# Optimization experiments

Measured on AMD Instinct MI355X. Metric: run time of the kernel, lower is better.

Reference implementation:

```python
import jax, jax.numpy as jnp
import numpy as np

# SREChead (single level, width=0.25): stem 1x1 (128->64) + two 3x3 convs (64->64),
# each Conv->BN(eval, folded into scale/shift)->SiLU, then 1x1 reg (4ch) and obj (1ch)
# heads, followed by YOLOX-style grid decode.
B, C_IN, HGT, WID = 64, 128, 80, 80
C_H = 64            # int(256 * 0.25)
STRIDE = 32


def _conv(x, w):
    # NCHW conv, stride 1, SAME padding (pad=(k-1)//2 as in BaseConv)
    return jax.lax.conv_general_dilated(
        x, w, window_strides=(1, 1), padding='SAME',
        dimension_numbers=('NCHW', 'OIHW', 'NCHW'))


def _bn_silu(y, scale, shift):
    # eval-mode BatchNorm folded to per-channel affine, then SiLU
    return jax.nn.silu(y * scale[None, :, None, None] + shift[None, :, None, None])


def setup_inputs() -> dict:
    key = jax.random.key(0)
    ks = jax.random.split(key, 12)

    def w(k, o, i, kh, kw, s=0.05):
        return jax.random.normal(k, (o, i, kh, kw), jnp.float32) * s

    def bn(k, c):
        k1, k2 = jax.random.split(k)
        scale = 1.0 + 0.1 * jax.random.normal(k1, (c,), jnp.float32)
        shift = 0.05 * jax.random.normal(k2, (c,), jnp.float32)
        return scale, shift

    stem_scale, stem_shift = bn(ks[2], C_H)
    c1_scale, c1_shift = bn(ks[4], C_H)
    c2_scale, c2_shift = bn(ks[6], C_H)
    return {
        'x': jax.random.normal(ks[0], (B, C_IN, HGT, WID), jnp.float32),
        'stem_w': w(ks[1], C_H, C_IN, 1, 1),
        'stem_scale': stem_scale, 'stem_shift': stem_shift,
        'c1_w': w(ks[3], C_H, C_H, 3, 3),
        'c1_scale': c1_scale, 'c1_shift': c1_shift,
        'c2_w': w(ks[5], C_H, C_H, 3, 3),
        'c2_scale': c2_scale, 'c2_shift': c2_shift,
        'reg_w': w(ks[7], 4, C_H, 1, 1),
        'reg_b': jnp.zeros((4,), jnp.float32),
        'obj_w': w(ks[8], 1, C_H, 1, 1),
        'obj_b': jnp.zeros((1,), jnp.float32),
    }


def reference(x, stem_w, stem_scale, stem_shift,
              c1_w, c1_scale, c1_shift,
              c2_w, c2_scale, c2_shift,
              reg_w, reg_b, obj_w, obj_b):
    f = _bn_silu(_conv(x, stem_w), stem_scale, stem_shift)       # [B,64,H,W]
    f = _bn_silu(_conv(f, c1_w), c1_scale, c1_shift)
    f = _bn_silu(_conv(f, c2_w), c2_scale, c2_shift)
    reg = _conv(f, reg_w) + reg_b[None, :, None, None]           # [B,4,H,W]
    obj = jax.nn.sigmoid(_conv(f, obj_w) + obj_b[None, :, None, None])  # [B,1,H,W]
    out = jnp.concatenate([reg, obj], axis=1)                    # [B,5,H,W]
    out = out.reshape(out.shape[0], 5, HGT * WID).transpose(0, 2, 1)  # [B,HW,5]
    # YOLOX decode: xy = (pred_xy + grid) * stride, wh = exp(pred_wh) * stride
    yv, xv = jnp.meshgrid(jnp.arange(HGT), jnp.arange(WID), indexing='ij')
    grid = jnp.stack([xv, yv], -1).reshape(1, HGT * WID, 2).astype(out.dtype)
    xy = (out[..., :2] + grid) * STRIDE
    wh = jnp.exp(out[..., 2:4]) * STRIDE
    return jnp.concatenate([xy, wh, out[..., 4:5]], axis=-1)     # [B,HW,5]
```

## Files before the change

kernel.cpp:

```cpp
#include <hip/hip_runtime.h>
#include <cstdint>


typedef short short8 __attribute__((ext_vector_type(8)));
typedef float floatx4 __attribute__((ext_vector_type(4)));

#define NPIX 6400
#define NBATCH 64

static __device__ __forceinline__ unsigned short f2bf(float f) {
    unsigned u = __builtin_bit_cast(unsigned, f);
    u += 0x7fffu + ((u >> 16) & 1u);
    return (unsigned short)(u >> 16);
}

static __device__ __forceinline__ float silu_(float v) {
    return v / (1.0f + __expf(-v));
}

__global__ __launch_bounds__(256) void rearr_w_kernel(
    const float* __restrict__ w1, const float* __restrict__ w2,
    unsigned short* __restrict__ wB1, unsigned short* __restrict__ wB2) {
    int idx = blockIdx.x * 256 + threadIdx.x;
    const float* src = (idx < 36864) ? w1 : w2;
    unsigned short* dst = (idx < 36864) ? wB1 : wB2;
    int e = (idx < 36864) ? idx : idx - 36864;
    int j = e & 7;
    int lane = (e >> 3) & 63;
    int nt = (e >> 9) & 3;
    int kb = e >> 11;
    int co = nt * 16 + (lane & 15);
    int k = kb * 32 + ((lane >> 4) * 8) + j;
    int ci = k & 63;
    int tap = k >> 6;
    dst[e] = f2bf(src[(co * 64 + ci) * 9 + tap]);
}

__global__ __launch_bounds__(256) void stem_kernel(
    const float* __restrict__ x, const float* __restrict__ w,
    const float* __restrict__ scale, const float* __restrict__ shift,
    unsigned short* __restrict__ f1) {
    int b = blockIdx.y;
    int wv = threadIdx.x >> 6;
    int lane = threadIdx.x & 63;
    int l15 = lane & 15, q = lane >> 4;
    int pbase = blockIdx.x * 256 + wv * 64;

    short8 wf[4][4];
    #pragma unroll
    for (int nt = 0; nt < 4; ++nt) {
        int co = nt * 16 + l15;
        #pragma unroll
        for (int kb = 0; kb < 4; ++kb) {
            const float* wp = w + co * 128 + kb * 32 + q * 8;
            short8 f;
            #pragma unroll
            for (int j = 0; j < 8; ++j) f[j] = (short)f2bf(wp[j]);
            wf[nt][kb] = f;
        }
    }
    float sc[4], sh[4];
    #pragma unroll
    for (int nt = 0; nt < 4; ++nt) {
        sc[nt] = scale[nt * 16 + l15];
        sh[nt] = shift[nt * 16 + l15];
    }

    floatx4 acc[4][4];
    floatx4 zf = {0.0f, 0.0f, 0.0f, 0.0f};
    #pragma unroll
    for (int mt = 0; mt < 4; ++mt)
        #pragma unroll
        for (int nt = 0; nt < 4; ++nt) acc[mt][nt] = zf;

    #pragma unroll
    for (int kb = 0; kb < 4; ++kb) {
        short8 af[4];
        #pragma unroll
        for (int mt = 0; mt < 4; ++mt) {
            int p = pbase + mt * 16 + l15;
            const float* xp = x + (b * 128 + kb * 32 + q * 8) * NPIX + p;
            short8 f;
            #pragma unroll
            for (int j = 0; j < 8; ++j) f[j] = (short)f2bf(xp[j * NPIX]);
            af[mt] = f;
        }
        #pragma unroll
        for (int mt = 0; mt < 4; ++mt)
            #pragma unroll
            for (int nt = 0; nt < 4; ++nt)
                acc[mt][nt] = __builtin_amdgcn_mfma_f32_16x16x32_bf16(
                    af[mt], wf[nt][kb], acc[mt][nt], 0, 0, 0);
    }

    #pragma unroll
    for (int mt = 0; mt < 4; ++mt) {
        #pragma unroll
        for (int nt = 0; nt < 4; ++nt) {
            int co = nt * 16 + l15;
            #pragma unroll
            for (int r = 0; r < 4; ++r) {
                int p = pbase + mt * 16 + q * 4 + r;
                float v = acc[mt][nt][r] * sc[nt] + sh[nt];
                f1[(b * NPIX + p) * 64 + co] = f2bf(silu_(v));
            }
        }
    }
}

__global__ __launch_bounds__(256) void conv3_kernel(
    const unsigned short* __restrict__ fin, const unsigned short* __restrict__ wB,
    const float* __restrict__ scale, const float* __restrict__ shift,
    unsigned short* __restrict__ fout) {
    int b = blockIdx.y;
    int wv = threadIdx.x >> 6;
    int lane = threadIdx.x & 63;
    int l15 = lane & 15, q = lane >> 4;
    int pbase = blockIdx.x * 256 + wv * 64;

    int py[4], pxl[4];
    #pragma unroll
    for (int mt = 0; mt < 4; ++mt) {
        int pt = pbase + mt * 16;
        py[mt] = pt / 80;
        pxl[mt] = pt % 80 + l15;
    }

    floatx4 acc[4][4];
    floatx4 zf = {0.0f, 0.0f, 0.0f, 0.0f};
    #pragma unroll
    for (int mt = 0; mt < 4; ++mt)
        #pragma unroll
        for (int nt = 0; nt < 4; ++nt) acc[mt][nt] = zf;

    const unsigned short* fb = fin + b * (NPIX * 64);

    for (int kb = 0; kb < 18; ++kb) {
        int tap = kb >> 1;
        int dy = tap / 3 - 1, dx = tap % 3 - 1;
        int ci0 = (kb & 1) * 32 + q * 8;
        short8 af[4];
        #pragma unroll
        for (int mt = 0; mt < 4; ++mt) {
            int yy = py[mt] + dy, xx = pxl[mt] + dx;
            short8 v = {};
            if ((unsigned)yy < 80u && (unsigned)xx < 80u)
                v = *(const short8*)(fb + (yy * 80 + xx) * 64 + ci0);
            af[mt] = v;
        }
        short8 bfr[4];
        #pragma unroll
        for (int nt = 0; nt < 4; ++nt)
            bfr[nt] = *(const short8*)(wB + ((kb * 4 + nt) * 64 + lane) * 8);
        #pragma unroll
        for (int mt = 0; mt < 4; ++mt)
            #pragma unroll
            for (int nt = 0; nt < 4; ++nt)
                acc[mt][nt] = __builtin_amdgcn_mfma_f32_16x16x32_bf16(
                    af[mt], bfr[nt], acc[mt][nt], 0, 0, 0);
    }

    float sc[4], sh[4];
    #pragma unroll
    for (int nt = 0; nt < 4; ++nt) {
        sc[nt] = scale[nt * 16 + l15];
        sh[nt] = shift[nt * 16 + l15];
    }
    #pragma unroll
    for (int mt = 0; mt < 4; ++mt) {
        #pragma unroll
        for (int nt = 0; nt < 4; ++nt) {
            int co = nt * 16 + l15;
            #pragma unroll
            for (int r = 0; r < 4; ++r) {
                int p = pbase + mt * 16 + q * 4 + r;
                float v = acc[mt][nt][r] * sc[nt] + sh[nt];
                fout[(b * NPIX + p) * 64 + co] = f2bf(silu_(v));
            }
        }
    }
}

__global__ __launch_bounds__(256) void conv_head_kernel(
    const unsigned short* __restrict__ fin, const unsigned short* __restrict__ wB,
    const float* __restrict__ scale, const float* __restrict__ shift,
    const float* __restrict__ reg_w, const float* __restrict__ reg_b,
    const float* __restrict__ obj_w, const float* __restrict__ obj_b,
    float* __restrict__ out) {
    __shared__ unsigned short h_lds[4][64 * 72];
    int b = blockIdx.y;
    int wv = threadIdx.x >> 6;
    int lane = threadIdx.x & 63;
    int l15 = lane & 15, q = lane >> 4;
    int pbase = blockIdx.x * 256 + wv * 64;

    int py[4], pxb[4];
    #pragma unroll
    for (int mt = 0; mt < 4; ++mt) {
        int pt = pbase + mt * 16;
        py[mt] = pt / 80;
        pxb[mt] = pt % 80;
    }

    floatx4 acc[4][4];
    floatx4 zf = {0.0f, 0.0f, 0.0f, 0.0f};
    #pragma unroll
    for (int mt = 0; mt < 4; ++mt)
        #pragma unroll
        for (int nt = 0; nt < 4; ++nt) acc[mt][nt] = zf;

    const unsigned short* fb = fin + b * (NPIX * 64);

    for (int kb = 0; kb < 18; ++kb) {
        int tap = kb >> 1;
        int dy = tap / 3 - 1, dx = tap % 3 - 1;
        int ci0 = (kb & 1) * 32 + q * 8;
        short8 af[4];
        #pragma unroll
        for (int mt = 0; mt < 4; ++mt) {
            int yy = py[mt] + dy, xx = pxb[mt] + l15 + dx;
            short8 v = {};
            if ((unsigned)yy < 80u && (unsigned)xx < 80u)
                v = *(const short8*)(fb + (yy * 80 + xx) * 64 + ci0);
            af[mt] = v;
        }
        short8 bfr[4];
        #pragma unroll
        for (int nt = 0; nt < 4; ++nt)
            bfr[nt] = *(const short8*)(wB + ((kb * 4 + nt) * 64 + lane) * 8);
        #pragma unroll
        for (int mt = 0; mt < 4; ++mt)
            #pragma unroll
            for (int nt = 0; nt < 4; ++nt)
                acc[mt][nt] = __builtin_amdgcn_mfma_f32_16x16x32_bf16(
                    af[mt], bfr[nt], acc[mt][nt], 0, 0, 0);
    }

    float sc[4], sh[4];
    #pragma unroll
    for (int nt = 0; nt < 4; ++nt) {
        sc[nt] = scale[nt * 16 + l15];
        sh[nt] = shift[nt * 16 + l15];
    }
    unsigned short* hp = h_lds[wv];
    #pragma unroll
    for (int mt = 0; mt < 4; ++mt) {
        #pragma unroll
        for (int nt = 0; nt < 4; ++nt) {
            int co = nt * 16 + l15;
            #pragma unroll
            for (int r = 0; r < 4; ++r) {
                int p_loc = mt * 16 + q * 4 + r;
                float v = acc[mt][nt][r] * sc[nt] + sh[nt];
                hp[p_loc * 72 + co] = f2bf(silu_(v));
            }
        }
    }
    __syncthreads();

    short8 hbf[2];
    #pragma unroll
    for (int kb2 = 0; kb2 < 2; ++kb2) {
        int k0 = kb2 * 32 + q * 8;
        short8 f = {};
        if (l15 < 4) {
            #pragma unroll
            for (int j = 0; j < 8; ++j) f[j] = (short)f2bf(reg_w[l15 * 64 + k0 + j]);
        } else if (l15 == 4) {
            #pragma unroll
            for (int j = 0; j < 8; ++j) f[j] = (short)f2bf(obj_w[k0 + j]);
        }
        hbf[kb2] = f;
    }

    floatx4 acc5[4];
    #pragma unroll
    for (int mt = 0; mt < 4; ++mt) acc5[mt] = zf;
    #pragma unroll
    for (int mt = 0; mt < 4; ++mt)
        #pragma unroll
        for (int kb2 = 0; kb2 < 2; ++kb2) {
            short8 a = *(const short8*)(hp + (mt * 16 + l15) * 72 + kb2 * 32 + q * 8);
            acc5[mt] = __builtin_amdgcn_mfma_f32_16x16x32_bf16(a, hbf[kb2], acc5[mt], 0, 0, 0);
        }

    float bias = 0.0f;
    if (l15 < 4) bias = reg_b[l15];
    else if (l15 == 4) bias = obj_b[0];

    #pragma unroll
    for (int mt = 0; mt < 4; ++mt) {
        #pragma unroll
        for (int r = 0; r < 4; ++r) {
            int p = pbase + mt * 16 + q * 4 + r;
            if (l15 < 5) {
                float v = acc5[mt][r] + bias;
                float gx = (float)(pxb[mt] + q * 4 + r);
                float gy = (float)py[mt];
                float o;
                if (l15 == 0)      o = (v + gx) * 32.0f;
                else if (l15 == 1) o = (v + gy) * 32.0f;
                else if (l15 < 4)  o = __expf(v) * 32.0f;
                else               o = 1.0f / (1.0f + __expf(-v));
                out[(b * NPIX + p) * 5 + l15] = o;
            }
        }
    }
}

extern "C" void kernel_launch(void* const* d_in, const int* in_sizes, int n_in,
                              void* d_out, int out_size, void* d_ws, size_t ws_size,
                              hipStream_t stream) {
    const float* x          = (const float*)d_in[0];
    const float* stem_w     = (const float*)d_in[1];
    const float* stem_scale = (const float*)d_in[2];
    const float* stem_shift = (const float*)d_in[3];
    const float* c1_w       = (const float*)d_in[4];
    const float* c1_scale   = (const float*)d_in[5];
    const float* c1_shift   = (const float*)d_in[6];
    const float* c2_w       = (const float*)d_in[7];
    const float* c2_scale   = (const float*)d_in[8];
    const float* c2_shift   = (const float*)d_in[9];
    const float* reg_w      = (const float*)d_in[10];
    const float* reg_b      = (const float*)d_in[11];
    const float* obj_w      = (const float*)d_in[12];
    const float* obj_b      = (const float*)d_in[13];
    float* out = (float*)d_out;

    const size_t needed = (size_t)(73728 + 2 * 64 * NPIX * 64) * 2;
    if (ws_size < needed) return;

    unsigned short* ws  = (unsigned short*)d_ws;
    unsigned short* wB1 = ws;
    unsigned short* wB2 = ws + 36864;
    unsigned short* f1  = ws + 73728;
    unsigned short* f2  = f1 + 64 * NPIX * 64;

    rearr_w_kernel<<<288, 256, 0, stream>>>(c1_w, c2_w, wB1, wB2);
    stem_kernel<<<dim3(25, 64), 256, 0, stream>>>(x, stem_w, stem_scale, stem_shift, f1);
    conv3_kernel<<<dim3(25, 64), 256, 0, stream>>>(f1, wB1, c1_scale, c1_shift, f2);
    conv_head_kernel<<<dim3(25, 64), 256, 0, stream>>>(f2, wB2, c2_scale, c2_shift,
                                                       reg_w, reg_b, obj_w, obj_b, out);
}
```

Baseline: 513.4 us.

## Use zero-padded NHWC feature buffers, swap MFMA operands, vectorize epilogue stores

Intermediate feature maps are now stored in 82x82 zero-bordered buffers, with the borders cleared by a new small kernel. This removes the per-load bounds checks and branches in both 3x3 convs. The MFMA operands are swapped so each lane holds four consecutive output channels of one pixel, which lets the BN+SiLU epilogue write 8-byte vector stores instead of scalar 2-byte ones. The tap loop is fully unrolled, and launch bounds request 3 blocks per CU. The tradeoff is a slightly larger workspace, one extra kernel launch, and possible register pressure from the full unroll.

Measured after the change: 543.1 us. 1.06x slower.

```diff
diff --git a/kernel.cpp b/kernel.cpp
--- a/kernel.cpp
+++ b/kernel.cpp
@@ -4,9 +4,11 @@
 
 typedef short short8 __attribute__((ext_vector_type(8)));
 typedef float floatx4 __attribute__((ext_vector_type(4)));
+typedef float fx4 __attribute__((ext_vector_type(4)));
+typedef unsigned short us4 __attribute__((ext_vector_type(4)));
 
 #define NPIX 6400
-#define NBATCH 64
+#define PADIMG (82 * 82 * 64)
 
 static __device__ __forceinline__ unsigned short f2bf(float f) {
     unsigned u = __builtin_bit_cast(unsigned, f);
@@ -27,19 +29,36 @@
     int e = (idx < 36864) ? idx : idx - 36864;
     int j = e & 7;
     int lane = (e >> 3) & 63;
-    int nt = (e >> 9) & 3;
+    int ct = (e >> 9) & 3;
     int kb = e >> 11;
-    int co = nt * 16 + (lane & 15);
+    int co = ct * 16 + (lane & 15);
     int k = kb * 32 + ((lane >> 4) * 8) + j;
     int ci = k & 63;
     int tap = k >> 6;
     dst[e] = f2bf(src[(co * 64 + ci) * 9 + tap]);
 }
 
+__global__ __launch_bounds__(256) void border_kernel(
+    unsigned short* __restrict__ f1p, unsigned short* __restrict__ f2p) {
+    int t = blockIdx.x * 256 + threadIdx.x;
+    int chunk = t % 5184;
+    int bb = t / 5184;
+    int buf = bb >> 6, b = bb & 63;
+    int pix = chunk >> 4;
+    int c4 = (chunk & 15) * 4;
+    int row, col;
+    if (pix < 82)       { row = 0;  col = pix; }
+    else if (pix < 164) { row = 81; col = pix - 82; }
+    else { int j = pix - 164; row = 1 + (j >> 1); col = (j & 1) * 81; }
+    unsigned short* base = (buf ? f2p : f1p) + (size_t)b * PADIMG + (row * 82 + col) * 64 + c4;
+    us4 z = {0, 0, 0, 0};
+    *(us4*)base = z;
+}
+
 __global__ __launch_bounds__(256) void stem_kernel(
     const float* __restrict__ x, const float* __restrict__ w,
     const float* __restrict__ scale, const float* __restrict__ shift,
-    unsigned short* __restrict__ f1) {
+    unsigned short* __restrict__ f1p) {
     int b = blockIdx.y;
     int wv = threadIdx.x >> 6;
     int lane = threadIdx.x & 63;
@@ -48,67 +67,74 @@
 
     short8 wf[4][4];
     #pragma unroll
-    for (int nt = 0; nt < 4; ++nt) {
-        int co = nt * 16 + l15;
+    for (int ct = 0; ct < 4; ++ct) {
+        int co = ct * 16 + l15;
         #pragma unroll
         for (int kb = 0; kb < 4; ++kb) {
             const float* wp = w + co * 128 + kb * 32 + q * 8;
+            fx4 a = *(const fx4*)wp;
+            fx4 bv = *(const fx4*)(wp + 4);
             short8 f;
             #pragma unroll
-            for (int j = 0; j < 8; ++j) f[j] = (short)f2bf(wp[j]);
-            wf[nt][kb] = f;
-        }
-    }
-    float sc[4], sh[4];
-    #pragma unroll
-    for (int nt = 0; nt < 4; ++nt) {
-        sc[nt] = scale[nt * 16 + l15];
-        sh[nt] = shift[nt * 16 + l15];
-    }
+            for (int j = 0; j < 4; ++j) f[j] = (short)f2bf(a[j]);
+            #pragma unroll
+            for (int j = 0; j < 4; ++j) f[j + 4] = (short)f2bf(bv[j]);
+            wf[ct][kb] = f;
+        }
+    }
+    float sc[4][4], sh[4][4];
+    #pragma unroll
+    for (int ct = 0; ct < 4; ++ct)
+        #pragma unroll
+        for (int r = 0; r < 4; ++r) {
+            sc[ct][r] = scale[ct * 16 + q * 4 + r];
+            sh[ct][r] = shift[ct * 16 + q * 4 + r];
+        }
 
     floatx4 acc[4][4];
     floatx4 zf = {0.0f, 0.0f, 0.0f, 0.0f};
     #pragma unroll
-    for (int mt = 0; mt < 4; ++mt)
-        #pragma unroll
-        for (int nt = 0; nt < 4; ++nt) acc[mt][nt] = zf;
+    for (int ct = 0; ct < 4; ++ct)
+        #pragma unroll
+        for (int pt = 0; pt < 4; ++pt) acc[ct][pt] = zf;
 
     #pragma unroll
     for (int kb = 0; kb < 4; ++kb) {
-        short8 af[4];
-        #pragma unroll
-        for (int mt = 0; mt < 4; ++mt) {
-            int p = pbase + mt * 16 + l15;
-            const float* xp = x + (b * 128 + kb * 32 + q * 8) * NPIX + p;
+        short8 xf[4];
+        #pragma unroll
+        for (int pt = 0; pt < 4; ++pt) {
+            int p = pbase + pt * 16 + l15;
+            const float* xp = x + (size_t)(b * 128 + kb * 32 + q * 8) * NPIX + p;
             short8 f;
             #pragma unroll
             for (int j = 0; j < 8; ++j) f[j] = (short)f2bf(xp[j * NPIX]);
-            af[mt] = f;
-        }
-        #pragma unroll
-        for (int mt = 0; mt < 4; ++mt)
-            #pragma unroll
-            for (int nt = 0; nt < 4; ++nt)
-                acc[mt][nt] = __builtin_amdgcn_mfma_f32_16x16x32_bf16(
-                    af[mt], wf[nt][kb], acc[mt][nt], 0, 0, 0);
-    }
-
-    #pragma unroll
-    for (int mt = 0; mt < 4; ++mt) {
-        #pragma unroll
-        for (int nt = 0; nt < 4; ++nt) {
-            int co = nt * 16 + l15;
-            #pragma unroll
-            for (int r = 0; r < 4; ++r) {
-                int p = pbase + mt * 16 + q * 4 + r;
-                float v = acc[mt][nt][r] * sc[nt] + sh[nt];
-                f1[(b * NPIX + p) * 64 + co] = f2bf(silu_(v));
-            }
-        }
-    }
-}
-
-__global__ __launch_bounds__(256) void conv3_kernel(
+            xf[pt] = f;
+        }
+        #pragma unroll
+        for (int ct = 0; ct < 4; ++ct)
+            #pragma unroll
+            for (int pt = 0; pt < 4; ++pt)
+                acc[ct][pt] = __builtin_amdgcn_mfma_f32_16x16x32_bf16(
+                    wf[ct][kb], xf[pt], acc[ct][pt], 0, 0, 0);
+    }
+
+    #pragma unroll
+    for (int pt = 0; pt < 4; ++pt) {
+        int p = pbase + pt * 16 + l15;
+        int y = p / 80, xc = p % 80;
+        unsigned short* dst = f1p + (size_t)b * PADIMG + ((y + 1) * 82 + (xc + 1)) * 64;
+        #pragma unroll
+        for (int ct = 0; ct < 4; ++ct) {
+            us4 v;
+            #pragma unroll
+            for (int r = 0; r < 4; ++r)
+                v[r] = f2bf(silu_(acc[ct][pt][r] * sc[ct][r] + sh[ct][r]));
+            *(us4*)(dst + ct * 16 + q * 4) = v;
+        }
+    }
+}
+
+__global__ __launch_bounds__(256, 3) void conv3_kernel(
     const unsigned short* __restrict__ fin, const unsigned short* __restrict__ wB,
     const float* __restrict__ scale, const float* __restrict__ shift,
     unsigned short* __restrict__ fout) {
@@ -118,70 +144,73 @@
     int l15 = lane & 15, q = lane >> 4;
     int pbase = blockIdx.x * 256 + wv * 64;
 
-    int py[4], pxl[4];
-    #pragma unroll
-    for (int mt = 0; mt < 4; ++mt) {
-        int pt = pbase + mt * 16;
-        py[mt] = pt / 80;
-        pxl[mt] = pt % 80 + l15;
+    int py[4], px0[4];
+    #pragma unroll
+    for (int pt = 0; pt < 4; ++pt) {
+        int pt16 = pbase + pt * 16;
+        py[pt] = pt16 / 80;
+        px0[pt] = pt16 % 80;
     }
 
     floatx4 acc[4][4];
     floatx4 zf = {0.0f, 0.0f, 0.0f, 0.0f};
     #pragma unroll
-    for (int mt = 0; mt < 4; ++mt)
-        #pragma unroll
-        for (int nt = 0; nt < 4; ++nt) acc[mt][nt] = zf;
-
-    const unsigned short* fb = fin + b * (NPIX * 64);
-
-    for (int kb = 0; kb < 18; ++kb) {
-        int tap = kb >> 1;
-        int dy = tap / 3 - 1, dx = tap % 3 - 1;
-        int ci0 = (kb & 1) * 32 + q * 8;
-        short8 af[4];
-        #pragma unroll
-        for (int mt = 0; mt < 4; ++mt) {
-            int yy = py[mt] + dy, xx = pxl[mt] + dx;
-            short8 v = {};
-            if ((unsigned)yy < 80u && (unsigned)xx < 80u)
-                v = *(const short8*)(fb + (yy * 80 + xx) * 64 + ci0);
-            af[mt] = v;
-        }
-        short8 bfr[4];
-        #pragma unroll
-        for (int nt = 0; nt < 4; ++nt)
-            bfr[nt] = *(const short8*)(wB + ((kb * 4 + nt) * 64 + lane) * 8);
-        #pragma unroll
-        for (int mt = 0; mt < 4; ++mt)
-            #pragma unroll
-            for (int nt = 0; nt < 4; ++nt)
-                acc[mt][nt] = __builtin_amdgcn_mfma_f32_16x16x32_bf16(
-                    af[mt], bfr[nt], acc[mt][nt], 0, 0, 0);
-    }
-
-    float sc[4], sh[4];
-    #pragma unroll
-    for (int nt = 0; nt < 4; ++nt) {
-        sc[nt] = scale[nt * 16 + l15];
-        sh[nt] = shift[nt * 16 + l15];
-    }
-    #pragma unroll
-    for (int mt = 0; mt < 4; ++mt) {
-        #pragma unroll
-        for (int nt = 0; nt < 4; ++nt) {
-            int co = nt * 16 + l15;
-            #pragma unroll
-            for (int r = 0; r < 4; ++r) {
-                int p = pbase + mt * 16 + q * 4 + r;
-                float v = acc[mt][nt][r] * sc[nt] + sh[nt];
-                fout[(b * NPIX + p) * 64 + co] = f2bf(silu_(v));
+    for (int ct = 0; ct < 4; ++ct)
+        #pragma unroll
+        for (int pt = 0; pt < 4; ++pt) acc[ct][pt] = zf;
+
+    const unsigned short* fb = fin + (size_t)b * PADIMG;
+
+    #pragma unroll
+    for (int tap = 0; tap < 9; ++tap) {
+        const int dy = tap / 3 - 1, dx = tap % 3 - 1;
+        #pragma unroll
+        for (int half = 0; half < 2; ++half) {
+            const int kb = tap * 2 + half;
+            short8 pf[4];
+            #pragma unroll
+            for (int pt = 0; pt < 4; ++pt) {
+                int addr = ((py[pt] + 1 + dy) * 82 + px0[pt] + l15 + 1 + dx) * 64
+                         + half * 32 + q * 8;
+                pf[pt] = *(const short8*)(fb + addr);
             }
-        }
-    }
-}
-
-__global__ __launch_bounds__(256) void conv_head_kernel(
+            short8 wf[4];
+            #pragma unroll
+            for (int ct = 0; ct < 4; ++ct)
+                wf[ct] = *(const short8*)(wB + ((kb * 4 + ct) * 64 + lane) * 8);
+            #pragma unroll
+            for (int ct = 0; ct < 4; ++ct)
+                #pragma unroll
+                for (int pt = 0; pt < 4; ++pt)
+                    acc[ct][pt] = __builtin_amdgcn_mfma_f32_16x16x32_bf16(
+                        wf[ct], pf[pt], acc[ct][pt], 0, 0, 0);
+        }
+    }
+
+    float sc[4][4], sh[4][4];
+    #pragma unroll
+    for (int ct = 0; ct < 4; ++ct)
+        #pragma unroll
+        for (int r = 0; r < 4; ++r) {
+            sc[ct][r] = scale[ct * 16 + q * 4 + r];
+            sh[ct][r] = shift[ct * 16 + q * 4 + r];
+        }
+    #pragma unroll
+    for (int pt = 0; pt < 4; ++pt) {
+        unsigned short* dst = fout + (size_t)b * PADIMG
+                            + ((py[pt] + 1) * 82 + px0[pt] + l15 + 1) * 64;
+        #pragma unroll
+        for (int ct = 0; ct < 4; ++ct) {
+            us4 v;
+            #pragma unroll
+            for (int r = 0; r < 4; ++r)
+                v[r] = f2bf(silu_(acc[ct][pt][r] * sc[ct][r] + sh[ct][r]));
+            *(us4*)(dst + ct * 16 + q * 4) = v;
+        }
+    }
+}
+
+__global__ __launch_bounds__(256, 3) void conv_head_kernel(
     const unsigned short* __restrict__ fin, const unsigned short* __restrict__ wB,
     const float* __restrict__ scale, const float* __restrict__ shift,
     const float* __restrict__ reg_w, const float* __restrict__ reg_b,
@@ -194,66 +223,67 @@
     int l15 = lane & 15, q = lane >> 4;
     int pbase = blockIdx.x * 256 + wv * 64;
 
-    int py[4], pxb[4];
-    #pragma unroll
-    for (int mt = 0; mt < 4; ++mt) {
-        int pt = pbase + mt * 16;
-        py[mt] = pt / 80;
-        pxb[mt] = pt % 80;
+    int py[4], px0[4];
+    #pragma unroll
+    for (int pt = 0; pt < 4; ++pt) {
+        int pt16 = pbase + pt * 16;
+        py[pt] = pt16 / 80;
+        px0[pt] = pt16 % 80;
     }
 
     floatx4 acc[4][4];
     floatx4 zf = {0.0f, 0.0f, 0.0f, 0.0f};
     #pragma unroll
-    for (int mt = 0; mt < 4; ++mt)
-        #pragma unroll
-        for (int nt = 0; nt < 4; ++nt) acc[mt][nt] = zf;
-
-    const unsigned short* fb = fin + b * (NPIX * 64);
-
-    for (int kb = 0; kb < 18; ++kb) {
-        int tap = kb >> 1;
-        int dy = tap / 3 - 1, dx = tap % 3 - 1;
-        int ci0 = (kb & 1) * 32 + q * 8;
-        short8 af[4];
-        #pragma unroll
-        for (int mt = 0; mt < 4; ++mt) {
-            int yy = py[mt] + dy, xx = pxb[mt] + l15 + dx;
-            short8 v = {};
-            if ((unsigned)yy < 80u && (unsigned)xx < 80u)
-                v = *(const short8*)(fb + (yy * 80 + xx) * 64 + ci0);
-            af[mt] = v;
-        }
-        short8 bfr[4];
-        #pragma unroll
-        for (int nt = 0; nt < 4; ++nt)
-            bfr[nt] = *(const short8*)(wB + ((kb * 4 + nt) * 64 + lane) * 8);
-        #pragma unroll
-        for (int mt = 0; mt < 4; ++mt)
-            #pragma unroll
-            for (int nt = 0; nt < 4; ++nt)
-                acc[mt][nt] = __builtin_amdgcn_mfma_f32_16x16x32_bf16(
-                    af[mt], bfr[nt], acc[mt][nt], 0, 0, 0);
-    }
-
-    float sc[4], sh[4];
-    #pragma unroll
-    for (int nt = 0; nt < 4; ++nt) {
-        sc[nt] = scale[nt * 16 + l15];
-        sh[nt] = shift[nt * 16 + l15];
-    }
+    for (int ct = 0; ct < 4; ++ct)
+        #pragma unroll
+        for (int pt = 0; pt < 4; ++pt) acc[ct][pt] = zf;
+
+    const unsigned short* fb = fin + (size_t)b * PADIMG;
+
+    #pragma unroll
+    for (int tap = 0; tap < 9; ++tap) {
+        const int dy = tap / 3 - 1, dx = tap % 3 - 1;
+        #pragma unroll
+        for (int half = 0; half < 2; ++half) {
+            const int kb = tap * 2 + half;
+            short8 pf[4];
+            #pragma unroll
+            for (int pt = 0; pt < 4; ++pt) {
+                int addr = ((py[pt] + 1 + dy) * 82 + px0[pt] + l15 + 1 + dx) * 64
+                         + half * 32 + q * 8;
+                pf[pt] = *(const short8*)(fb + addr);
+            }
+            short8 wf[4];
+            #pragma unroll
+            for (int ct = 0; ct < 4; ++ct)
+                wf[ct] = *(const short8*)(wB + ((kb * 4 + ct) * 64 + lane) * 8);
+            #pragma unroll
+            for (int ct = 0; ct < 4; ++ct)
+                #pragma unroll
+                for (int pt = 0; pt < 4; ++pt)
+                    acc[ct][pt] = __builtin_amdgcn_mfma_f32_16x16x32_bf16(
+                        wf[ct], pf[pt], acc[ct][pt], 0, 0, 0);
+        }
+    }
+
+    float sc[4][4], sh[4][4];
+    #pragma unroll
+    for (int ct = 0; ct < 4; ++ct)
+        #pragma unroll
+        for (int r = 0; r < 4; ++r) {
+            sc[ct][r] = scale[ct * 16 + q * 4 + r];
+            sh[ct][r] = shift[ct * 16 + q * 4 + r];
+        }
     unsigned short* hp = h_lds[wv];
     #pragma unroll
-    for (int mt = 0; mt < 4; ++mt) {
-        #pragma unroll
-        for (int nt = 0; nt < 4; ++nt) {
-            int co = nt * 16 + l15;
-            #pragma unroll
-            for (int r = 0; r < 4; ++r) {
-                int p_loc = mt * 16 + q * 4 + r;
-                float v = acc[mt][nt][r] * sc[nt] + sh[nt];
-                hp[p_loc * 72 + co] = f2bf(silu_(v));
-            }
+    for (int pt = 0; pt < 4; ++pt) {
+        #pragma unroll
+        for (int ct = 0; ct < 4; ++ct) {
+            us4 v;
+            #pragma unroll
+            for (int r = 0; r < 4; ++r)
+                v[r] = f2bf(silu_(acc[ct][pt][r] * sc[ct][r] + sh[ct][r]));
+            *(us4*)(hp + (pt * 16 + l15) * 72 + ct * 16 + q * 4) = v;
         }
     }
     __syncthreads();
@@ -295,14 +325,14 @@
             int p = pbase + mt * 16 + q * 4 + r;
             if (l15 < 5) {
                 float v = acc5[mt][r] + bias;
-                float gx = (float)(pxb[mt] + q * 4 + r);
+                float gx = (float)(px0[mt] + q * 4 + r);
                 float gy = (float)py[mt];
                 float o;
                 if (l15 == 0)      o = (v + gx) * 32.0f;
                 else if (l15 == 1) o = (v + gy) * 32.0f;
                 else if (l15 < 4)  o = __expf(v) * 32.0f;
                 else               o = 1.0f / (1.0f + __expf(-v));
-                out[(b * NPIX + p) * 5 + l15] = o;
+                out[(size_t)(b * NPIX + p) * 5 + l15] = o;
             }
         }
     }
@@ -327,18 +357,19 @@
     const float* obj_b      = (const float*)d_in[13];
     float* out = (float*)d_out;
 
-    const size_t needed = (size_t)(73728 + 2 * 64 * NPIX * 64) * 2;
+    const size_t needed = ((size_t)73728 + 2 * (size_t)64 * PADIMG) * 2;
     if (ws_size < needed) return;
 
     unsigned short* ws  = (unsigned short*)d_ws;
     unsigned short* wB1 = ws;
     unsigned short* wB2 = ws + 36864;
-    unsigned short* f1  = ws + 73728;
-    unsigned short* f2  = f1 + 64 * NPIX * 64;
+    unsigned short* f1p = ws + 73728;
+    unsigned short* f2p = f1p + (size_t)64 * PADIMG;
 
     rearr_w_kernel<<<288, 256, 0, stream>>>(c1_w, c2_w, wB1, wB2);
-    stem_kernel<<<dim3(25, 64), 256, 0, stream>>>(x, stem_w, stem_scale, stem_shift, f1);
-    conv3_kernel<<<dim3(25, 64), 256, 0, stream>>>(f1, wB1, c1_scale, c1_shift, f2);
-    conv_head_kernel<<<dim3(25, 64), 256, 0, stream>>>(f2, wB2, c2_scale, c2_shift,
+    border_kernel<<<2592, 256, 0, stream>>>(f1p, f2p);
+    stem_kernel<<<dim3(25, 64), 256, 0, stream>>>(x, stem_w, stem_scale, stem_shift, f1p);
+    conv3_kernel<<<dim3(25, 64), 256, 0, stream>>>(f1p, wB1, c1_scale, c1_shift, f2p);
+    conv_head_kernel<<<dim3(25, 64), 256, 0, stream>>>(f2p, wB2, c2_scale, c2_shift,
                                                        reg_w, reg_b, obj_w, obj_b, out);
 }
```
